# Kernel optimization log

Hardware: AMD Instinct MI355X
Metric: run time of the kernel (lower is better)

The kernel has to match this reference:

```python
import jax, jax.numpy as jnp
import numpy as np

D_MODEL = 64; D_INNER = 64; D_STATE = 8; DT_RANK = 4; D_CONV = 4
B, C, H, W = 16, 1024, 32, 32


def _silu(x):
    return x * jax.nn.sigmoid(x)


def _layernorm(x, g, b, eps=1e-5):
    m = x.mean(-1, keepdims=True)
    v = ((x - m) ** 2).mean(-1, keepdims=True)
    return (x - m) * jax.lax.rsqrt(v + eps) * g + b


def _rmsnorm(x, w, eps=1e-5):
    return x * jax.lax.rsqrt((x * x).mean(-1, keepdims=True) + eps) * w


def _causal_conv1d(x, w, b):
    # x: [B, D, L]; depthwise causal conv, kernel w: [D, K]
    D = x.shape[1]; K = w.shape[1]
    xp = jnp.pad(x, ((0, 0), (0, 0), (K - 1, 0)))
    y = jax.lax.conv_general_dilated(xp, w[:, None, :], (1,), 'VALID',
                                     dimension_numbers=('NCH', 'OIH', 'NCH'),
                                     feature_group_count=D)
    return y + b[None, :, None]


def _selective_scan(x, z, A_log, Dvec, xproj_w, dt_w, dt_b):
    # x, z: [B, D, L]
    A = -jnp.exp(A_log)                                    # [D, N]
    xdb = jnp.einsum('bdl,kd->blk', x, xproj_w)            # [B, L, R+2N]
    dt_lr = xdb[..., :DT_RANK]
    Bc = xdb[..., DT_RANK:DT_RANK + D_STATE]               # [B, L, N]
    Cc = xdb[..., DT_RANK + D_STATE:]                      # [B, L, N]
    dt = jax.nn.softplus(jnp.einsum('blr,dr->bld', dt_lr, dt_w) + dt_b)  # [B, L, D]
    dA = jnp.exp(dt[..., None] * A[None, None])            # [B, L, D, N]
    dBx = dt[..., None] * Bc[:, :, None, :] * x.transpose(0, 2, 1)[..., None]  # [B, L, D, N]

    def step(h, inp):
        dA_t, dBx_t, C_t = inp
        h = dA_t * h + dBx_t                               # [B, D, N]
        return h, jnp.einsum('bdn,bn->bd', h, C_t)

    h0 = jnp.zeros((x.shape[0], x.shape[1], D_STATE), x.dtype)
    _, ys = jax.lax.scan(step, h0, (dA.transpose(1, 0, 2, 3),
                                    dBx.transpose(1, 0, 2, 3),
                                    Cc.transpose(1, 0, 2)))
    y = ys.transpose(1, 2, 0) + Dvec[None, :, None] * x    # [B, D, L]
    return y * _silu(z)


def _mamba_branch(u, in_w, conv_w, conv_b, xproj_w, dt_w, dt_b, A_log, Dvec):
    # u: [B, L, d_model]
    xz = jnp.einsum('bld,ed->bel', u, in_w)                # [B, 2*D_INNER, L]
    x, z = jnp.split(xz, 2, axis=1)
    x = _silu(_causal_conv1d(x, conv_w, conv_b))
    return _selective_scan(x, z, A_log, Dvec, xproj_w, dt_w, dt_b)


def setup_inputs():
    key = jax.random.key(0)
    ks = jax.random.split(key, 20)
    rn = lambda i, shape, s=1.0: jax.random.normal(ks[i], shape, dtype=jnp.float32) * s
    s4d = jnp.log(jnp.tile(jnp.arange(1, D_STATE + 1, dtype=jnp.float32)[None, :], (D_INNER, 1)))
    return {
        'img1': rn(0, (B, C, H, W)),
        'img2': rn(1, (B, C, H, W)),
        'pre_w': rn(2, (D_MODEL, 1), 0.3),
        'pre_b': rn(3, (D_MODEL,), 0.1),
        'ln_g': jnp.ones((D_MODEL,), jnp.float32),
        'ln_b': jnp.zeros((D_MODEL,), jnp.float32),
        'in_w': rn(4, (2 * D_INNER, D_MODEL), 0.1),
        'in_b_w': rn(5, (2 * D_INNER, D_MODEL), 0.1),
        'conv_w': rn(6, (D_INNER, D_CONV), 0.3),
        'conv_bias': rn(7, (D_INNER,), 0.1),
        'convb_w': rn(8, (D_INNER, D_CONV), 0.3),
        'convb_bias': rn(9, (D_INNER,), 0.1),
        'xproj_w': rn(10, (DT_RANK + 2 * D_STATE, D_INNER), 0.1),
        'xprojb_w': rn(11, (DT_RANK + 2 * D_STATE, D_INNER), 0.1),
        'dt_w': rn(12, (D_INNER, DT_RANK), 0.1),
        'dt_bias': rn(13, (D_INNER,), 0.1),
        'dtb_w': rn(14, (D_INNER, DT_RANK), 0.1),
        'dtb_bias': rn(15, (D_INNER,), 0.1),
        'A_log': s4d,
        'A_b_log': s4d,
        'Dp': jnp.ones((D_INNER,), jnp.float32),
        'Dp_b': jnp.ones((D_INNER,), jnp.float32),
        'norm_w': jnp.ones((D_INNER,), jnp.float32),
        'out_w': rn(16, (D_MODEL, D_INNER), 0.1),
        'post_w': rn(17, (1, D_MODEL), 0.3),
        'post_b': jnp.zeros((1,), jnp.float32),
    }


def reference(img1, img2, pre_w, pre_b, ln_g, ln_b, in_w, in_b_w, conv_w, conv_bias,
              convb_w, convb_bias, xproj_w, xprojb_w, dt_w, dt_bias, dtb_w, dtb_bias,
              A_log, A_b_log, Dp, Dp_b, norm_w, out_w, post_w, post_b):
    # AdaptiveMaxPool2d((1,1)) + squeeze(-1) -> [B, C, 1]
    p1 = jnp.max(img1, axis=(2, 3))[..., None]
    p2 = jnp.max(img2, axis=(2, 3))[..., None]
    # pre_linear: Linear(1, 64) then LayerNorm(64)  -> [B, C(=L), 64]
    x1 = _layernorm(p1 * pre_w[:, 0] + pre_b, ln_g, ln_b)
    x2 = _layernorm(p2 * pre_w[:, 0] + pre_b, ln_g, ln_b)
    # bimamba v3 (cross): forward scan on x1, reversed scan on extra_emb=x2
    out_f = _mamba_branch(x1, in_w, conv_w, conv_bias, xproj_w, dt_w, dt_bias, A_log, Dp)
    out_b = _mamba_branch(x2[:, ::-1, :], in_b_w, convb_w, convb_bias, xprojb_w,
                          dtb_w, dtb_bias, A_b_log, Dp_b)[:, :, ::-1]
    y = (out_f + out_b).transpose(0, 2, 1)                 # [B, L, D_INNER]
    y = _rmsnorm(y, norm_w)                                # use_norm=True
    y = jnp.einsum('bld,ed->ble', y, out_w)                # out_proj (no bias)
    att = jnp.einsum('bld,od->blo', y, post_w) + post_b    # post_linear -> [B, C, 1]
    return jax.nn.sigmoid(att[..., None])                  # [B, C, 1, 1]
```

## Files before the change

kernel.cpp:

```cpp
#include <hip/hip_runtime.h>
#include <math.h>

typedef float f32x4 __attribute__((ext_vector_type(4)));

#define NCH 32
#define CLN 32

#define OFF_P   0
#define OFF_Q   524288
#define OFF_DTT 1048576
#define OFF_SXT 3145728
#define OFF_BCT 5242880
#define OFF_AN  5767168
#define OFF_HIN 5832704
#define OFF_WZ  6356992
#define OFF_VEW 6357376
#define OFF_AL2 6357440

#define LOG2E 1.4426950408889634f
#define LN2   0.6931471805599453f

__device__ __forceinline__ float fexp2(float x){ return __builtin_amdgcn_exp2f(x); }
__device__ __forceinline__ float flog2(float x){ return __builtin_amdgcn_logf(x); }
__device__ __forceinline__ float frcp (float x){ return __builtin_amdgcn_rcpf(x); }
__device__ __forceinline__ float fsigmoid(float x){ return frcp(1.f + fexp2(-x*LOG2E)); }
__device__ __forceinline__ float fsilu(float x){ return x * fsigmoid(x); }
__device__ __forceinline__ float fsoftplus(float x){
  return fmaxf(x, 0.f) + LN2 * flog2(1.f + fexp2(-fabsf(x)*LOG2E));
}

__device__ __forceinline__ float wave_rsum(float v){
  #pragma unroll
  for (int o = 1; o < 64; o <<= 1) v += __shfl_xor(v, o, 64);
  return v;
}
__device__ __forceinline__ float wave_rmax(float v){
  #pragma unroll
  for (int o = 1; o < 64; o <<= 1) v = fmaxf(v, __shfl_xor(v, o, 64));
  return v;
}

struct Smem {
  float a1[36], a2[36], a3[36];
  float xpt[20*65];
  float dtlr[32*4];
  float sxt[64*37];
  float dtt[32*64];
  float bct[32*16];
  float gw[64], gb[64], lnbs[64];
  float W[384];
  float cst[4];
};

__device__ __forceinline__ void consts_ln(float* gw, float* gb, float* lnbs, float* cst, int t,
    const float* pre_w, const float* pre_b, const float* ln_g, const float* ln_b){
  if (t < 64){
    float w = pre_w[t], b = pre_b[t];
    float mw = wave_rsum(w) * (1.f/64.f);
    float mb = wave_rsum(b) * (1.f/64.f);
    float wc = w - mw, bc = b - mb;
    float Av = wave_rsum(wc*wc) * (1.f/64.f);
    float Bq = wave_rsum(wc*bc) * (1.f/64.f);
    float Cq = wave_rsum(bc*bc) * (1.f/64.f);
    gw[t] = wc * ln_g[t];
    gb[t] = bc * ln_g[t];
    lnbs[t] = ln_b[t];
    if (t == 0){ cst[0] = Av; cst[1] = Bq; cst[2] = Cq; }
  }
}

__device__ __forceinline__ void proj_body(
    Smem& S, int t,
    const float* __restrict__ cw, const float* __restrict__ cb,
    const float* __restrict__ xpw, const float* __restrict__ dw,
    const float* __restrict__ dbv){
  for (int i = t; i < 20*64; i += 512){
    int k = i >> 6, d = i & 63;
    S.xpt[k*65 + d] = xpw[i];
  }
  __syncthreads();
  {
    int d = t & 63, lq = t >> 6;
    float cw0=cw[d*4], cw1=cw[d*4+1], cw2=cw[d*4+2], cw3=cw[d*4+3];
    float cbd = cb[d];
    float W1d = S.W[d], W2d = S.W[128+d], W3d = S.W[256+d];
    #pragma unroll
    for (int j = 0; j < 4; ++j){
      int ll = lq*4 + j;
      float A1 = cw0*S.a1[ll] + cw1*S.a1[ll+1] + cw2*S.a1[ll+2] + cw3*S.a1[ll+3];
      float A2 = cw0*S.a2[ll] + cw1*S.a2[ll+1] + cw2*S.a2[ll+2] + cw3*S.a2[ll+3];
      float A3 = cw0*S.a3[ll] + cw1*S.a3[ll+1] + cw2*S.a3[ll+2] + cw3*S.a3[ll+3];
      float xc = W1d*A1 + W2d*A2 + W3d*A3 + cbd;
      S.sxt[d*37 + ll] = fsilu(xc);
    }
  }
  __syncthreads();
  {
    int ll = t >> 4, k = t & 15;
    float acc = 0.f;
    #pragma unroll 8
    for (int d = 0; d < 64; ++d) acc += S.xpt[(4+k)*65 + d] * S.sxt[d*37 + ll];
    S.bct[ll*16 + k] = acc;
  }
  if (t < 128){
    int ll = t >> 2, r = t & 3;
    float acc = 0.f;
    #pragma unroll 8
    for (int d = 0; d < 64; ++d) acc += S.xpt[r*65 + d] * S.sxt[d*37 + ll];
    S.dtlr[ll*4 + r] = acc;
  }
  __syncthreads();
  {
    int d = t & 63, lq = t >> 6;
    float w0=dw[d*4], w1=dw[d*4+1], w2=dw[d*4+2], w3=dw[d*4+3];
    float bd = dbv[d];
    #pragma unroll
    for (int j = 0; j < 4; ++j){
      int ll = lq*4 + j;
      float raw = bd + w0*S.dtlr[ll*4] + w1*S.dtlr[ll*4+1]
                     + w2*S.dtlr[ll*4+2] + w3*S.dtlr[ll*4+3];
      S.dtt[ll*64 + d] = fsoftplus(raw);
    }
  }
  __syncthreads();
}

__global__ void __launch_bounds__(512) k_projA(
    const float* __restrict__ img1, const float* __restrict__ img2,
    const float* pre_w, const float* pre_b, const float* ln_g, const float* ln_b,
    const float* in_w, const float* in_b_w, const float* A_log, const float* A_b_log,
    const float* conv_w, const float* conv_b, const float* convb_w, const float* convb_b,
    const float* xproj_w, const float* xprojb_w,
    const float* dt_w, const float* dt_b, const float* dtb_w, const float* dtb_b,
    const float* norm_w, const float* out_w, const float* post_w,
    float* __restrict__ ws){
  __shared__ __align__(16) Smem S;
  int bi = blockIdx.x;
  int c = bi & 31, bq = bi >> 5, br = bq >> 4, b = bq & 15;
  int t = threadIdx.x;
  int wv = t >> 6, lane = t & 63;
  const float* img = br ? img2 : img1;
  #pragma unroll
  for (int k = 0; k < 5; ++k){
    int i = wv + k*8;
    if (i < 35){
      bool valid = (c > 0) || (i >= 3);
      if (valid){
        int l = br ? (1026 - c*32 - i) : (c*32 - 3 + i);
        const f32x4* rp = (const f32x4*)(img + ((size_t)(b*1024 + l))*1024) + lane;
        f32x4 q0 = __builtin_nontemporal_load(rp +   0);
        f32x4 q1 = __builtin_nontemporal_load(rp +  64);
        f32x4 q2 = __builtin_nontemporal_load(rp + 128);
        f32x4 q3 = __builtin_nontemporal_load(rp + 192);
        float m = fmaxf(fmaxf(fmaxf(q0.x,q0.y), fmaxf(q0.z,q0.w)),
                        fmaxf(fmaxf(q1.x,q1.y), fmaxf(q1.z,q1.w)));
        m = fmaxf(m, fmaxf(fmaxf(fmaxf(q2.x,q2.y), fmaxf(q2.z,q2.w)),
                           fmaxf(fmaxf(q3.x,q3.y), fmaxf(q3.z,q3.w))));
        m = wave_rmax(m);
        if (lane == 0) S.a1[i] = m;
      } else if (lane == 0) S.a1[i] = 0.f;
    }
  }
  consts_ln(S.gw, S.gb, S.lnbs, S.cst, t, pre_w, pre_b, ln_g, ln_b);
  __syncthreads();
  if (t < 128){
    const float* iw = br ? in_b_w : in_w;
    float s1 = 0.f, s2 = 0.f, s3 = 0.f;
    #pragma unroll 8
    for (int d = 0; d < 64; ++d){
      float w = iw[t*64 + d];
      s1 += w * S.gw[d]; s2 += w * S.gb[d]; s3 += w * S.lnbs[d];
    }
    S.W[      t] = s1;
    S.W[128 + t] = s2;
    S.W[256 + t] = s3;
  }
  float A2r = -fexp2((br ? A_b_log : A_log)[t] * LOG2E) * LOG2E;
  __syncthreads();
  if (t < 36){
    bool ok = (t < 35) && ((c > 0) || (t >= 3));
    float m = ok ? S.a1[t] : 0.f;
    float Av = S.cst[0], Bq = S.cst[1], Cq = S.cst[2];
    float inv = rsqrtf(m*m*Av + 2.f*m*Bq + Cq + 1e-5f);
    S.a1[t] = ok ? m*inv : 0.f;
    S.a2[t] = ok ? inv   : 0.f;
    S.a3[t] = ok ? 1.f   : 0.f;
  }
  proj_body(S, t,
            br ? convb_w : conv_w,  br ? convb_b : conv_b,
            br ? xprojb_w : xproj_w, br ? dtb_w : dt_w, br ? dtb_b : dt_b);
  {
    int dd = t >> 3, tt0 = (t & 7)*4;
    f32x4 sv; sv.x = S.sxt[dd*37+tt0];   sv.y = S.sxt[dd*37+tt0+1];
              sv.z = S.sxt[dd*37+tt0+2]; sv.w = S.sxt[dd*37+tt0+3];
    *(f32x4*)(ws + OFF_SXT + (size_t)bi*2048 + dd*32 + tt0) = sv;
    f32x4 dv; dv.x = S.dtt[t*4];   dv.y = S.dtt[t*4+1];
              dv.z = S.dtt[t*4+2]; dv.w = S.dtt[t*4+3];
    *(f32x4*)(ws + OFF_DTT + (size_t)bi*2048 + t*4) = dv;
    if (t < 128){
      f32x4 bv; bv.x = S.bct[t*4];   bv.y = S.bct[t*4+1];
                bv.z = S.bct[t*4+2]; bv.w = S.bct[t*4+3];
      *(f32x4*)(ws + OFF_BCT + (size_t)bi*512 + t*4) = bv;
    }
    if (t < 32){
      ws[OFF_AN + (size_t)bi*64 + t]      = S.a1[t+3];
      ws[OFF_AN + (size_t)bi*64 + 32 + t] = S.a2[t+3];
    }
  }
  if (bi == 0 || bi == 512){
    ws[OFF_AL2 + br*512 + t] = A2r;
    if (t < 64){
      ws[OFF_WZ + br*192 +       t] = S.W[64 + t];
      ws[OFF_WZ + br*192 +  64 + t] = S.W[128 + 64 + t];
      ws[OFF_WZ + br*192 + 128 + t] = S.W[256 + 64 + t];
    }
    if (bi == 0 && t < 64){
      float s = 0.f;
      #pragma unroll 8
      for (int e = 0; e < 64; ++e) s += post_w[e] * out_w[e*64 + t];
      ws[OFF_VEW + t] = s * norm_w[t];
    }
  }
  int d = wv*8 + (lane >> 3), n = lane & 7;
  float P = 1.f, Q = 0.f;
  #pragma unroll 4
  for (int tt = 0; tt < CLN; ++tt){
    float dtv = S.dtt[tt*64 + d];
    float xv  = S.sxt[d*37 + tt];
    float bv  = S.bct[tt*16 + n];
    float da  = fexp2(dtv * A2r);
    Q = fmaf(da, Q, dtv * bv * xv);
    P *= da;
  }
  ws[OFF_P + (size_t)bi*512 + t] = P;
  ws[OFF_Q + (size_t)bi*512 + t] = Q;
}

__global__ void __launch_bounds__(64) k_scanB(float* __restrict__ ws){
  int gid = blockIdx.x*64 + threadIdx.x;
  int bq = gid >> 9, dn = gid & 511;
  size_t base = (size_t)bq*NCH*512 + dn;
  float P[NCH], Q[NCH];
  #pragma unroll
  for (int c = 0; c < NCH; ++c){
    P[c] = ws[OFF_P + base + (size_t)c*512];
    Q[c] = ws[OFF_Q + base + (size_t)c*512];
  }
  float h = 0.f;
  #pragma unroll
  for (int c = 0; c < NCH; ++c){
    ws[OFF_HIN + base + (size_t)c*512] = h;
    h = fmaf(P[c], h, Q[c]);
  }
}

__global__ void __launch_bounds__(512) k_scanY(
    const float* Dp, const float* Dp_b, const float* post_b,
    const float* __restrict__ ws, float* __restrict__ out){
  __shared__ __align__(16) struct {
    float dtt[2][2048];
    float sxt[2][2368];
    float bct[2][512];
    float an[2][64];
    float ylds[CLN*65];
  } C;
  int bi = blockIdx.x;
  int oc = bi & 31, b = bi >> 5;
  int t = threadIdx.x;
  int lane = t & 63, wv = t >> 6;
  int d = wv*8 + (lane >> 3), n = lane & 7;
  int ti0 = b*32 + oc;
  int ti1 = (b+16)*32 + (31 - oc);
  f32x4 dv0 = *(const f32x4*)(ws + OFF_DTT + (size_t)ti0*2048 + t*4);
  f32x4 dv1 = *(const f32x4*)(ws + OFF_DTT + (size_t)ti1*2048 + t*4);
  f32x4 sv0 = *(const f32x4*)(ws + OFF_SXT + (size_t)ti0*2048 + t*4);
  f32x4 sv1 = *(const f32x4*)(ws + OFF_SXT + (size_t)ti1*2048 + t*4);
  float h0  = ws[OFF_HIN + (size_t)ti0*512 + t];
  float h1  = ws[OFF_HIN + (size_t)ti1*512 + t];
  float A2r0 = ws[OFF_AL2 +       t];
  float A2r1 = ws[OFF_AL2 + 512 + t];
  float W1z0 = ws[OFF_WZ +       d], W2z0 = ws[OFF_WZ +  64 + d], W3z0 = ws[OFF_WZ + 128 + d];
  float W1z1 = ws[OFF_WZ + 192 + d], W2z1 = ws[OFF_WZ + 256 + d], W3z1 = ws[OFF_WZ + 320 + d];
  float Dp0 = Dp[d], Dp1 = Dp_b[d];
  float ve = ws[OFF_VEW + lane];
  float pb = post_b[0];
  f32x4 bv0, bv1, av0, av1;
  if (t < 128){
    bv0 = *(const f32x4*)(ws + OFF_BCT + (size_t)ti0*512 + t*4);
    bv1 = *(const f32x4*)(ws + OFF_BCT + (size_t)ti1*512 + t*4);
  }
  if (t < 16){
    av0 = *(const f32x4*)(ws + OFF_AN + (size_t)ti0*64 + t*4);
    av1 = *(const f32x4*)(ws + OFF_AN + (size_t)ti1*64 + t*4);
  }
  {
    *(f32x4*)&C.dtt[0][t*4] = dv0;
    *(f32x4*)&C.dtt[1][t*4] = dv1;
    int dd = t >> 3, tt0 = (t & 7)*4;
    C.sxt[0][dd*37+tt0+0] = sv0.x; C.sxt[0][dd*37+tt0+1] = sv0.y;
    C.sxt[0][dd*37+tt0+2] = sv0.z; C.sxt[0][dd*37+tt0+3] = sv0.w;
    C.sxt[1][dd*37+tt0+0] = sv1.x; C.sxt[1][dd*37+tt0+1] = sv1.y;
    C.sxt[1][dd*37+tt0+2] = sv1.z; C.sxt[1][dd*37+tt0+3] = sv1.w;
    if (t < 128){
      *(f32x4*)&C.bct[0][t*4] = bv0;
      *(f32x4*)&C.bct[1][t*4] = bv1;
    }
    if (t < 16){
      *(f32x4*)&C.an[0][t*4] = av0;
      *(f32x4*)&C.an[1][t*4] = av1;
    }
  }
  __syncthreads();
  #pragma unroll
  for (int pass = 0; pass < 2; ++pass){
    float h   = pass ? h1 : h0;
    float A2r = pass ? A2r1 : A2r0;
    float Dpd = pass ? Dp1 : Dp0;
    float W1z = pass ? W1z1 : W1z0;
    float W2z = pass ? W2z1 : W2z0;
    float W3z = pass ? W3z1 : W3z0;
    const float* dtt = C.dtt[pass];
    const float* sxt = C.sxt[pass];
    const float* bct = C.bct[pass];
    const float* an  = C.an[pass];
    #pragma unroll 4
    for (int tt = 0; tt < CLN; ++tt){
      float dtv = dtt[tt*64 + d];
      float xv  = sxt[d*37 + tt];
      float bv  = bct[tt*16 + n];
      float cv  = bct[tt*16 + 8 + n];
      float da  = fexp2(dtv * A2r);
      h = fmaf(da, h, dtv * bv * xv);
      float pv = h * cv;
      pv += __shfl_xor(pv, 1, 64);
      pv += __shfl_xor(pv, 2, 64);
      pv += __shfl_xor(pv, 4, 64);
      if (n == 0){
        float y = pv + Dpd * xv;
        float zv = an[tt]*W1z + an[32+tt]*W2z + W3z;
        float g = fsilu(zv);
        int row = pass ? (31 - tt) : tt;
        if (pass == 0) C.ylds[row*65 + d] = y * g;
        else           C.ylds[row*65 + d] += y * g;
      }
    }
  }
  __syncthreads();
  #pragma unroll
  for (int j = 0; j < 4; ++j){
    int row = wv*4 + j;
    float v = C.ylds[row*65 + lane];
    float ss = v*v, dp = v*ve;
    #pragma unroll
    for (int o = 1; o < 64; o <<= 1){
      ss += __shfl_xor(ss, o, 64);
      dp += __shfl_xor(dp, o, 64);
    }
    if (lane == 0){
      float rstd = rsqrtf(ss*(1.f/64.f) + 1e-5f);
      out[b*1024 + oc*32 + row] = fsigmoid(dp*rstd + pb);
    }
  }
}

extern "C" void kernel_launch(void* const* d_in, const int* in_sizes, int n_in,
                              void* d_out, int out_size, void* d_ws, size_t ws_size,
                              hipStream_t stream){
  const float* img1      = (const float*)d_in[0];
  const float* img2      = (const float*)d_in[1];
  const float* pre_w     = (const float*)d_in[2];
  const float* pre_b     = (const float*)d_in[3];
  const float* ln_g      = (const float*)d_in[4];
  const float* ln_b      = (const float*)d_in[5];
  const float* in_w      = (const float*)d_in[6];
  const float* in_b_w    = (const float*)d_in[7];
  const float* conv_w    = (const float*)d_in[8];
  const float* conv_bias = (const float*)d_in[9];
  const float* convb_w   = (const float*)d_in[10];
  const float* convb_bias= (const float*)d_in[11];
  const float* xproj_w   = (const float*)d_in[12];
  const float* xprojb_w  = (const float*)d_in[13];
  const float* dt_w      = (const float*)d_in[14];
  const float* dt_bias   = (const float*)d_in[15];
  const float* dtb_w     = (const float*)d_in[16];
  const float* dtb_bias  = (const float*)d_in[17];
  const float* A_log     = (const float*)d_in[18];
  const float* A_b_log   = (const float*)d_in[19];
  const float* Dp        = (const float*)d_in[20];
  const float* Dp_b      = (const float*)d_in[21];
  const float* norm_w    = (const float*)d_in[22];
  const float* out_w     = (const float*)d_in[23];
  const float* post_w    = (const float*)d_in[24];
  const float* post_b    = (const float*)d_in[25];
  float* ws  = (float*)d_ws;
  float* out = (float*)d_out;

  k_projA<<<1024, 512, 0, stream>>>(img1, img2, pre_w, pre_b, ln_g, ln_b,
                                    in_w, in_b_w, A_log, A_b_log,
                                    conv_w, conv_bias, convb_w, convb_bias,
                                    xproj_w, xprojb_w, dt_w, dt_bias, dtb_w, dtb_bias,
                                    norm_w, out_w, post_w, ws);
  k_scanB<<<256, 64, 0, stream>>>(ws);
  k_scanY<<<512, 512, 0, stream>>>(Dp, Dp_b, post_b, ws, out);
}
```

Before: 71.29 us.

## Fuse chunk-carry scan into projA via last-block atomic; split scanY into two teams

Removes the separate k_scanB launch. The last block of each batch/branch group, detected with an atomic counter, performs the inter-chunk carry scan inside k_projA. k_scanY now runs 1024 threads so the forward and reverse branches scan concurrently in two teams instead of two sequential passes, then sums both buffers. This adds a memset launch, an atomic and a fence, and a serial tail in the last block of each group.

```diff
diff --git a/kernel.cpp b/kernel.cpp
--- a/kernel.cpp
+++ b/kernel.cpp
@@ -16,6 +16,7 @@
 #define OFF_WZ  6356992
 #define OFF_VEW 6357376
 #define OFF_AL2 6357440
+#define OFF_CNT 6358464
 
 #define LOG2E 1.4426950408889634f
 #define LN2   0.6931471805599453f
@@ -135,6 +136,7 @@
     const float* norm_w, const float* out_w, const float* post_w,
     float* __restrict__ ws){
   __shared__ __align__(16) Smem S;
+  __shared__ unsigned s_last;
   int bi = blockIdx.x;
   int c = bi & 31, bq = bi >> 5, br = bq >> 4, b = bq & 15;
   int t = threadIdx.x;
@@ -234,27 +236,39 @@
   }
   ws[OFF_P + (size_t)bi*512 + t] = P;
   ws[OFF_Q + (size_t)bi*512 + t] = Q;
-}
-
-__global__ void __launch_bounds__(64) k_scanB(float* __restrict__ ws){
-  int gid = blockIdx.x*64 + threadIdx.x;
-  int bq = gid >> 9, dn = gid & 511;
-  size_t base = (size_t)bq*NCH*512 + dn;
-  float P[NCH], Q[NCH];
-  #pragma unroll
-  for (int c = 0; c < NCH; ++c){
-    P[c] = ws[OFF_P + base + (size_t)c*512];
-    Q[c] = ws[OFF_Q + base + (size_t)c*512];
-  }
-  float h = 0.f;
-  #pragma unroll
-  for (int c = 0; c < NCH; ++c){
-    ws[OFF_HIN + base + (size_t)c*512] = h;
-    h = fmaf(P[c], h, Q[c]);
-  }
-}
-
-__global__ void __launch_bounds__(512) k_scanY(
+  __syncthreads();
+  if (t == 0){
+    __threadfence();
+    unsigned* cnt = (unsigned*)(ws + OFF_CNT);
+    unsigned old = __hip_atomic_fetch_add(&cnt[bq], 1u, __ATOMIC_ACQ_REL,
+                                          __HIP_MEMORY_SCOPE_AGENT);
+    s_last = (old == 31u) ? 1u : 0u;
+  }
+  __syncthreads();
+  if (s_last){
+    __threadfence();
+    const float* Pp = ws + OFF_P + (size_t)bq*NCH*512 + t;
+    const float* Qp = ws + OFF_Q + (size_t)bq*NCH*512 + t;
+    float* Hp = ws + OFF_HIN + (size_t)bq*NCH*512 + t;
+    float h = 0.f;
+    #pragma unroll
+    for (int base = 0; base < NCH; base += 8){
+      float Pa[8], Qa[8];
+      #pragma unroll
+      for (int j = 0; j < 8; ++j){
+        Pa[j] = Pp[(size_t)(base+j)*512];
+        Qa[j] = Qp[(size_t)(base+j)*512];
+      }
+      #pragma unroll
+      for (int j = 0; j < 8; ++j){
+        Hp[(size_t)(base+j)*512] = h;
+        h = fmaf(Pa[j], h, Qa[j]);
+      }
+    }
+  }
+}
+
+__global__ void __launch_bounds__(1024) k_scanY(
     const float* Dp, const float* Dp_b, const float* post_b,
     const float* __restrict__ ws, float* __restrict__ out){
   __shared__ __align__(16) struct {
@@ -262,67 +276,44 @@
     float sxt[2][2368];
     float bct[2][512];
     float an[2][64];
-    float ylds[CLN*65];
+    float ylds[2][CLN*65];
   } C;
   int bi = blockIdx.x;
   int oc = bi & 31, b = bi >> 5;
   int t = threadIdx.x;
-  int lane = t & 63, wv = t >> 6;
-  int d = wv*8 + (lane >> 3), n = lane & 7;
-  int ti0 = b*32 + oc;
-  int ti1 = (b+16)*32 + (31 - oc);
-  f32x4 dv0 = *(const f32x4*)(ws + OFF_DTT + (size_t)ti0*2048 + t*4);
-  f32x4 dv1 = *(const f32x4*)(ws + OFF_DTT + (size_t)ti1*2048 + t*4);
-  f32x4 sv0 = *(const f32x4*)(ws + OFF_SXT + (size_t)ti0*2048 + t*4);
-  f32x4 sv1 = *(const f32x4*)(ws + OFF_SXT + (size_t)ti1*2048 + t*4);
-  float h0  = ws[OFF_HIN + (size_t)ti0*512 + t];
-  float h1  = ws[OFF_HIN + (size_t)ti1*512 + t];
-  float A2r0 = ws[OFF_AL2 +       t];
-  float A2r1 = ws[OFF_AL2 + 512 + t];
-  float W1z0 = ws[OFF_WZ +       d], W2z0 = ws[OFF_WZ +  64 + d], W3z0 = ws[OFF_WZ + 128 + d];
-  float W1z1 = ws[OFF_WZ + 192 + d], W2z1 = ws[OFF_WZ + 256 + d], W3z1 = ws[OFF_WZ + 320 + d];
-  float Dp0 = Dp[d], Dp1 = Dp_b[d];
-  float ve = ws[OFF_VEW + lane];
-  float pb = post_b[0];
-  f32x4 bv0, bv1, av0, av1;
-  if (t < 128){
-    bv0 = *(const f32x4*)(ws + OFF_BCT + (size_t)ti0*512 + t*4);
-    bv1 = *(const f32x4*)(ws + OFF_BCT + (size_t)ti1*512 + t*4);
-  }
-  if (t < 16){
-    av0 = *(const f32x4*)(ws + OFF_AN + (size_t)ti0*64 + t*4);
-    av1 = *(const f32x4*)(ws + OFF_AN + (size_t)ti1*64 + t*4);
-  }
-  {
-    *(f32x4*)&C.dtt[0][t*4] = dv0;
-    *(f32x4*)&C.dtt[1][t*4] = dv1;
-    int dd = t >> 3, tt0 = (t & 7)*4;
-    C.sxt[0][dd*37+tt0+0] = sv0.x; C.sxt[0][dd*37+tt0+1] = sv0.y;
-    C.sxt[0][dd*37+tt0+2] = sv0.z; C.sxt[0][dd*37+tt0+3] = sv0.w;
-    C.sxt[1][dd*37+tt0+0] = sv1.x; C.sxt[1][dd*37+tt0+1] = sv1.y;
-    C.sxt[1][dd*37+tt0+2] = sv1.z; C.sxt[1][dd*37+tt0+3] = sv1.w;
-    if (t < 128){
-      *(f32x4*)&C.bct[0][t*4] = bv0;
-      *(f32x4*)&C.bct[1][t*4] = bv1;
-    }
-    if (t < 16){
-      *(f32x4*)&C.an[0][t*4] = av0;
-      *(f32x4*)&C.an[1][t*4] = av1;
-    }
-  }
-  __syncthreads();
-  #pragma unroll
-  for (int pass = 0; pass < 2; ++pass){
-    float h   = pass ? h1 : h0;
-    float A2r = pass ? A2r1 : A2r0;
-    float Dpd = pass ? Dp1 : Dp0;
-    float W1z = pass ? W1z1 : W1z0;
-    float W2z = pass ? W2z1 : W2z0;
-    float W3z = pass ? W3z1 : W3z0;
-    const float* dtt = C.dtt[pass];
-    const float* sxt = C.sxt[pass];
-    const float* bct = C.bct[pass];
-    const float* an  = C.an[pass];
+  int team = t >> 9, u = t & 511;
+  int lane = t & 63;
+  int wv_all = t >> 6;
+  int d = ((u >> 6) << 3) + ((u & 63) >> 3), n = u & 7;
+  int ti = team ? ((b+16)*32 + (31 - oc)) : (b*32 + oc);
+  f32x4 dv = *(const f32x4*)(ws + OFF_DTT + (size_t)ti*2048 + u*4);
+  f32x4 sv = *(const f32x4*)(ws + OFF_SXT + (size_t)ti*2048 + u*4);
+  float h   = ws[OFF_HIN + (size_t)ti*512 + u];
+  float A2r = ws[OFF_AL2 + team*512 + u];
+  float W1z = ws[OFF_WZ + team*192 +       d];
+  float W2z = ws[OFF_WZ + team*192 +  64 + d];
+  float W3z = ws[OFF_WZ + team*192 + 128 + d];
+  float Dpd = (team ? Dp_b : Dp)[d];
+  float ve  = ws[OFF_VEW + lane];
+  float pb  = post_b[0];
+  f32x4 bv4, av4;
+  if (u < 128) bv4 = *(const f32x4*)(ws + OFF_BCT + (size_t)ti*512 + u*4);
+  if (u < 16)  av4 = *(const f32x4*)(ws + OFF_AN  + (size_t)ti*64  + u*4);
+  {
+    *(f32x4*)&C.dtt[team][u*4] = dv;
+    int dd = u >> 3, tt0 = (u & 7)*4;
+    C.sxt[team][dd*37+tt0+0] = sv.x; C.sxt[team][dd*37+tt0+1] = sv.y;
+    C.sxt[team][dd*37+tt0+2] = sv.z; C.sxt[team][dd*37+tt0+3] = sv.w;
+    if (u < 128) *(f32x4*)&C.bct[team][u*4] = bv4;
+    if (u < 16)  *(f32x4*)&C.an[team][u*4]  = av4;
+  }
+  __syncthreads();
+  {
+    const float* dtt = C.dtt[team];
+    const float* sxt = C.sxt[team];
+    const float* bct = C.bct[team];
+    const float* an  = C.an[team];
+    float* yl = C.ylds[team];
     #pragma unroll 4
     for (int tt = 0; tt < CLN; ++tt){
       float dtv = dtt[tt*64 + d];
@@ -339,17 +330,16 @@
         float y = pv + Dpd * xv;
         float zv = an[tt]*W1z + an[32+tt]*W2z + W3z;
         float g = fsilu(zv);
-        int row = pass ? (31 - tt) : tt;
-        if (pass == 0) C.ylds[row*65 + d] = y * g;
-        else           C.ylds[row*65 + d] += y * g;
+        int row = team ? (31 - tt) : tt;
+        yl[row*65 + d] = y * g;
       }
     }
   }
   __syncthreads();
   #pragma unroll
-  for (int j = 0; j < 4; ++j){
-    int row = wv*4 + j;
-    float v = C.ylds[row*65 + lane];
+  for (int j = 0; j < 2; ++j){
+    int row = wv_all*2 + j;
+    float v = C.ylds[0][row*65 + lane] + C.ylds[1][row*65 + lane];
     float ss = v*v, dp = v*ve;
     #pragma unroll
     for (int o = 1; o < 64; o <<= 1){
@@ -395,11 +385,11 @@
   float* ws  = (float*)d_ws;
   float* out = (float*)d_out;
 
+  hipMemsetAsync((void*)(ws + OFF_CNT), 0, NCH*sizeof(unsigned), stream);
   k_projA<<<1024, 512, 0, stream>>>(img1, img2, pre_w, pre_b, ln_g, ln_b,
                                     in_w, in_b_w, A_log, A_b_log,
                                     conv_w, conv_bias, convb_w, convb_bias,
                                     xproj_w, xprojb_w, dt_w, dt_bias, dtb_w, dtb_bias,
                                     norm_w, out_w, post_w, ws);
-  k_scanB<<<256, 64, 0, stream>>>(ws);
-  k_scanY<<<512, 512, 0, stream>>>(Dp, Dp_b, post_b, ws, out);
-}
+  k_scanY<<<512, 1024, 0, stream>>>(Dp, Dp_b, post_b, ws, out);
+}
```

Result: slower. 163.1 us (+128.8%).
